# Optimization experiments

Measured on AMD Instinct MI355X. Metric: run time of the kernel, lower is better.

The kernel has to match this reference:

```python
import jax, jax.numpy as jnp
import numpy as np

N = 50000      # nodes
E = 800000     # directed edges (before self-loops)
IN = 128       # in_channels
H = 4          # heads (layers 1,2)
C = 64         # hidden_channels per head
OUT = 512      # out_channels of final Linear
LEAKY_SLOPE = 0.2


def _gat_layer(x, src, dst, n, W, a_src, a_dst, b, concat):
    """PyG GATConv (v1): shared linear, additive attention, segment softmax over dst."""
    heads, ch = a_src.shape
    xl = (x @ W).reshape(n, heads, ch)                       # [N,H,C]
    as_n = jnp.sum(xl * a_src, axis=-1)                      # [N,H] alpha_src per node
    ad_n = jnp.sum(xl * a_dst, axis=-1)                      # [N,H] alpha_dst per node
    logits = jax.nn.leaky_relu(as_n[src] + ad_n[dst], LEAKY_SLOPE)  # [Etot,H]
    m = jax.lax.stop_gradient(jax.ops.segment_max(logits, dst, num_segments=n))
    p = jnp.exp(logits - m[dst])
    denom = jax.ops.segment_sum(p, dst, num_segments=n) + 1e-16
    alpha = p / denom[dst]                                   # segment softmax over incoming edges
    out = jax.ops.segment_sum(xl[src] * alpha[:, :, None], dst, num_segments=n)  # [N,H,C]
    out = out.reshape(n, heads * ch) if concat else out.mean(axis=1)
    return out + b


def setup_inputs() -> dict:
    key = jax.random.key(0)
    ks = jax.random.split(key, 16)

    def gl(k, shape, fan_in):
        return jax.random.normal(k, shape, dtype=jnp.float32) * np.float32(1.0 / np.sqrt(fan_in))

    x = jax.random.normal(ks[0], (N, IN), dtype=jnp.float32)
    edge_index = jax.random.randint(ks[1], (2, E), 0, N, dtype=jnp.int32)

    inp = {
        "x": x,
        "edge_index": edge_index,
        # layer 1: in -> H*C (concat)
        "W1": gl(ks[2], (IN, H * C), IN),
        "a_src1": gl(ks[3], (H, C), C),
        "a_dst1": gl(ks[4], (H, C), C),
        "b1": jnp.zeros((H * C,), jnp.float32),
        # layer 2: H*C -> H*C (concat)
        "W2": gl(ks[5], (H * C, H * C), H * C),
        "a_src2": gl(ks[6], (H, C), C),
        "a_dst2": gl(ks[7], (H, C), C),
        "b2": jnp.zeros((H * C,), jnp.float32),
        # layer 3: H*C -> C (1 head, no concat)
        "W3": gl(ks[8], (H * C, C), H * C),
        "a_src3": gl(ks[9], (1, C), C),
        "a_dst3": gl(ks[10], (1, C), C),
        "b3": jnp.zeros((C,), jnp.float32),
        # final fc: C -> OUT
        "Wfc": gl(ks[11], (C, OUT), C),
        "bfc": jnp.zeros((OUT,), jnp.float32),
    }
    return inp


def reference(x, edge_index, W1, a_src1, a_dst1, b1, W2, a_src2, a_dst2, b2,
              W3, a_src3, a_dst3, b3, Wfc, bfc):
    n = x.shape[0]
    loop = jnp.arange(n, dtype=edge_index.dtype)             # PyG GATConv adds self-loops
    src = jnp.concatenate([edge_index[0], loop])
    dst = jnp.concatenate([edge_index[1], loop])

    h = jax.nn.relu(_gat_layer(x, src, dst, n, W1, a_src1, a_dst1, b1, True))
    h = jax.nn.relu(_gat_layer(h, src, dst, n, W2, a_src2, a_dst2, b2, True))
    h = jax.nn.relu(_gat_layer(h, src, dst, n, W3, a_src3, a_dst3, b3, False))
    return jax.nn.relu(h @ Wfc + bfc)                        # [N, OUT]
```

## Files before the change

kernel.cpp:

```cpp
#include <hip/hip_runtime.h>
#include <cstdint>
#include <cstddef>

typedef unsigned short ushort_t;
typedef __bf16 bf16x8 __attribute__((ext_vector_type(8)));
typedef float f32x4 __attribute__((ext_vector_type(4)));

__device__ __forceinline__ float b2f(ushort_t u) {
    return __uint_as_float(((unsigned int)u) << 16);
}
__device__ __forceinline__ ushort_t f2b(float f) {
    __bf16 h = (__bf16)f;
    return *(ushort_t*)&h;
}
__device__ __forceinline__ float lo16(unsigned int u) { return __uint_as_float(u << 16); }
__device__ __forceinline__ float hi16(unsigned int u) { return __uint_as_float(u & 0xffff0000u); }
__device__ __forceinline__ unsigned int pack2(float a, float b) {
    return ((unsigned int)f2b(b) << 16) | (unsigned int)f2b(a);
}

__device__ __forceinline__ void tr_seg(int id, const float* __restrict__ W,
                                       ushort_t* __restrict__ WT, int K, int N2) {
    int n = id / K, k = id - n * K;
    WT[id] = f2b(W[k * N2 + n]);
}
__global__ __launch_bounds__(256) void transpose_all_kernel(const float* __restrict__ W1,
                                                            const float* __restrict__ W2,
                                                            const float* __restrict__ W3,
                                                            const float* __restrict__ Wfc,
                                                            ushort_t* __restrict__ W1T,
                                                            ushort_t* __restrict__ W2T,
                                                            ushort_t* __restrict__ W3T,
                                                            ushort_t* __restrict__ WfcT) {
    int id = blockIdx.x * 256 + threadIdx.x;
    if (id < 32768) { tr_seg(id, W1, W1T, 128, 256); return; }
    id -= 32768;
    if (id < 65536) { tr_seg(id, W2, W2T, 256, 256); return; }
    id -= 65536;
    if (id < 16384) { tr_seg(id, W3, W3T, 256, 64); return; }
    id -= 16384;
    if (id < 32768) { tr_seg(id, Wfc, WfcT, 64, 512); return; }
}

__global__ __launch_bounds__(256) void xb_kernel(const float* __restrict__ x,
                                                 ushort_t* __restrict__ xb, int total8) {
    int id = blockIdx.x * 256 + threadIdx.x;
    if (id >= total8) return;
    const float* g = x + (size_t)id * 8;
    float4 f0 = *(const float4*)g;
    float4 f1 = *(const float4*)(g + 4);
    uint4 o;
    o.x = pack2(f0.x, f0.y); o.y = pack2(f0.z, f0.w);
    o.z = pack2(f1.x, f1.y); o.w = pack2(f1.z, f1.w);
    ((uint4*)xb)[id] = o;
}

__global__ __launch_bounds__(256) void degree_kernel(const int* __restrict__ ei_dst,
                                                     int* __restrict__ deg, int E, int Etot) {
    int e = blockIdx.x * 256 + threadIdx.x;
    if (e >= Etot) return;
    int d = (e < E) ? ei_dst[e] : (e - E);
    atomicAdd(&deg[d], 1);
}

__global__ __launch_bounds__(256) void partial_sum_kernel(const int* __restrict__ deg,
                                                          int* __restrict__ bsum, int n) {
    __shared__ int ws[4];
    int t = threadIdx.x;
    int i = blockIdx.x * 256 + t;
    int v = (i < n) ? deg[i] : 0;
#pragma unroll
    for (int off = 32; off; off >>= 1) v += __shfl_xor(v, off, 64);
    if ((t & 63) == 0) ws[t >> 6] = v;
    __syncthreads();
    if (t == 0) bsum[blockIdx.x] = ws[0] + ws[1] + ws[2] + ws[3];
}

__global__ __launch_bounds__(256) void scan_bsum_kernel(const int* __restrict__ bsum,
                                                        int* __restrict__ boff,
                                                        int* __restrict__ rowoff,
                                                        int nblk, int n) {
    __shared__ int sm[256];
    int t = threadIdx.x;
    int v = (t < nblk) ? bsum[t] : 0;
    sm[t] = v;
    __syncthreads();
#pragma unroll
    for (int off = 1; off < 256; off <<= 1) {
        int u = (t >= off) ? sm[t - off] : 0;
        __syncthreads();
        sm[t] += u;
        __syncthreads();
    }
    if (t < nblk) boff[t] = sm[t] - v;
    if (t == 255) rowoff[n] = sm[255];
}

__global__ __launch_bounds__(256) void block_scan_kernel(const int* __restrict__ deg,
                                                         const int* __restrict__ boff,
                                                         int* __restrict__ rowoff,
                                                         int* __restrict__ cursor, int n) {
    __shared__ int sm[256];
    int t = threadIdx.x;
    int i = blockIdx.x * 256 + t;
    int v = (i < n) ? deg[i] : 0;
    sm[t] = v;
    __syncthreads();
#pragma unroll
    for (int off = 1; off < 256; off <<= 1) {
        int u = (t >= off) ? sm[t - off] : 0;
        __syncthreads();
        sm[t] += u;
        __syncthreads();
    }
    if (i < n) {
        int r = boff[blockIdx.x] + sm[t] - v;
        rowoff[i] = r;
        cursor[i] = r;
    }
}

__global__ __launch_bounds__(256) void scatter_kernel(const int* __restrict__ ei_src,
                                                      const int* __restrict__ ei_dst,
                                                      int* __restrict__ cursor,
                                                      int* __restrict__ ssrc, int E, int Etot) {
    int e = blockIdx.x * 256 + threadIdx.x;
    if (e >= Etot) return;
    int s, d;
    if (e < E) { s = ei_src[e]; d = ei_dst[e]; } else { s = d = e - E; }
    int pos = atomicAdd(&cursor[d], 1);
    ssrc[pos] = s;
}

template <int EPI>
__global__ __launch_bounds__(256) void gemm128_mfma(const ushort_t* __restrict__ A,
                                                    const ushort_t* __restrict__ WT,
                                                    float* __restrict__ C,
                                                    ushort_t* __restrict__ Cb,
                                                    const float* __restrict__ bias,
                                                    int M, int K, int N2) {
    __shared__ ushort_t sA[128 * 32];
    __shared__ ushort_t sB[128 * 32];
    const int tid = threadIdx.x;
    const int wv = tid >> 6, lane = tid & 63;
    const int wr = wv >> 1, wc = wv & 1;
    const int quad = lane >> 4, l16 = lane & 15;
    const int bm = blockIdx.x * 128, bn = blockIdx.y * 128;
    const int sr0 = tid >> 2, sc = (tid & 3) * 8;
    const int sr1 = sr0 + 64;
    f32x4 acc[4][4] = {};

    int ga0 = bm + sr0; ga0 = ga0 < M ? ga0 : M - 1;
    int ga1 = bm + sr1; ga1 = ga1 < M ? ga1 : M - 1;
    const ushort_t* pa0 = A + (size_t)ga0 * K + sc;
    const ushort_t* pa1 = A + (size_t)ga1 * K + sc;
    const ushort_t* pb0 = WT + (size_t)(bn + sr0) * K + sc;
    const ushort_t* pb1 = WT + (size_t)(bn + sr1) * K + sc;

    for (int k0 = 0; k0 < K; k0 += 32) {
        *(float4*)(sA + sr0 * 32 + sc) = *(const float4*)(pa0 + k0);
        *(float4*)(sA + sr1 * 32 + sc) = *(const float4*)(pa1 + k0);
        *(float4*)(sB + sr0 * 32 + sc) = *(const float4*)(pb0 + k0);
        *(float4*)(sB + sr1 * 32 + sc) = *(const float4*)(pb1 + k0);
        __syncthreads();

        bf16x8 af[4], bfr[4];
#pragma unroll
        for (int m = 0; m < 4; m++)
            af[m] = *(const bf16x8*)(sA + (wr * 64 + m * 16 + l16) * 32 + quad * 8);
#pragma unroll
        for (int n = 0; n < 4; n++)
            bfr[n] = *(const bf16x8*)(sB + (wc * 64 + n * 16 + l16) * 32 + quad * 8);
#pragma unroll
        for (int m = 0; m < 4; m++)
#pragma unroll
            for (int n = 0; n < 4; n++)
                acc[m][n] = __builtin_amdgcn_mfma_f32_16x16x32_bf16(af[m], bfr[n], acc[m][n], 0, 0, 0);
        __syncthreads();
    }

#pragma unroll
    for (int n = 0; n < 4; n++) {
        int col = bn + wc * 64 + n * 16 + l16;
        float bv = (EPI == 1) ? bias[col] : 0.f;
#pragma unroll
        for (int m = 0; m < 4; m++) {
#pragma unroll
            for (int r = 0; r < 4; r++) {
                int row = bm + wr * 64 + m * 16 + quad * 4 + r;
                if (row < M) {
                    float v = acc[m][n][r];
                    if (EPI == 1) {
                        v += bv;
                        v = v > 0.f ? v : 0.f;
                        C[(size_t)row * N2 + col] = v;
                    } else {
                        Cb[(size_t)row * N2 + col] = f2b(v);
                    }
                }
            }
        }
    }
}

__global__ __launch_bounds__(256) void gemm64_mfma(const ushort_t* __restrict__ A,
                                                   const ushort_t* __restrict__ WT,
                                                   ushort_t* __restrict__ Cb,
                                                   int M, int K, int N2) {
    __shared__ ushort_t sA[64 * 32];
    __shared__ ushort_t sB[64 * 32];
    const int tid = threadIdx.x;
    const int wv = tid >> 6, lane = tid & 63;
    const int quad = lane >> 4, l16 = lane & 15;
    const int bm = blockIdx.x * 64;
    const int srow = tid >> 2, skof = (tid & 3) * 8;
    f32x4 acc[4] = {};

    int gm = bm + srow;
    gm = gm < M ? gm : M - 1;
    const ushort_t* pa = A + (size_t)gm * K + skof;
    const ushort_t* pb = WT + (size_t)srow * K + skof;

    for (int k0 = 0; k0 < K; k0 += 32) {
        *(float4*)(sA + srow * 32 + skof) = *(const float4*)(pa + k0);
        *(float4*)(sB + srow * 32 + skof) = *(const float4*)(pb + k0);
        __syncthreads();

        bf16x8 af = *(const bf16x8*)(sA + (wv * 16 + l16) * 32 + quad * 8);
#pragma unroll
        for (int j = 0; j < 4; j++) {
            bf16x8 bf = *(const bf16x8*)(sB + (j * 16 + l16) * 32 + quad * 8);
            acc[j] = __builtin_amdgcn_mfma_f32_16x16x32_bf16(af, bf, acc[j], 0, 0, 0);
        }
        __syncthreads();
    }

#pragma unroll
    for (int j = 0; j < 4; j++) {
        int col = j * 16 + l16;
#pragma unroll
        for (int r = 0; r < 4; r++) {
            int row = bm + wv * 16 + quad * 4 + r;
            if (row < M) Cb[(size_t)row * N2 + col] = f2b(acc[j][r]);
        }
    }
}

template <int CH>
__global__ __launch_bounds__(256) void attn_kernel(const ushort_t* __restrict__ xl,
                                                   const float* __restrict__ a_src,
                                                   const float* __restrict__ a_dst,
                                                   float* __restrict__ as_n,
                                                   float* __restrict__ ad_n, int N) {
    int n = blockIdx.x * 4 + (threadIdx.x >> 6);
    int lane = threadIdx.x & 63;
    if (n >= N) return;
    if (CH == 256) {
        ushort4 u = ((const ushort4*)xl)[(size_t)n * 64 + lane];
        float4 av = ((const float4*)a_src)[lane];
        float4 dv = ((const float4*)a_dst)[lane];
        float x0 = b2f(u.x), x1 = b2f(u.y), x2 = b2f(u.z), x3 = b2f(u.w);
        float s = x0 * av.x + x1 * av.y + x2 * av.z + x3 * av.w;
        float d = x0 * dv.x + x1 * dv.y + x2 * dv.z + x3 * dv.w;
#pragma unroll
        for (int off = 8; off; off >>= 1) {
            s += __shfl_xor(s, off, 64);
            d += __shfl_xor(d, off, 64);
        }
        if ((lane & 15) == 0) {
            int h = lane >> 4;
            as_n[n * 4 + h] = s;
            ad_n[n * 4 + h] = d;
        }
    } else {
        float xv = b2f(xl[(size_t)n * 64 + lane]);
        float s = xv * a_src[lane];
        float d = xv * a_dst[lane];
#pragma unroll
        for (int off = 32; off; off >>= 1) {
            s += __shfl_xor(s, off, 64);
            d += __shfl_xor(d, off, 64);
        }
        if (lane == 0) { as_n[n] = s; ad_n[n] = d; }
    }
}

template <int CH>
__global__ __launch_bounds__(256) void aggregate_kernel(const ushort_t* __restrict__ xl,
                                                        const float* __restrict__ as_n,
                                                        const float* __restrict__ ad_n,
                                                        const int* __restrict__ rowoff,
                                                        const int* __restrict__ ssrc,
                                                        const float* __restrict__ bias,
                                                        ushort_t* __restrict__ hout, int N) {
    const int tid = threadIdx.x;
    const int wv = tid >> 6, lane = tid & 63;
    const uint4* xv = (const uint4*)xl;
    if (CH == 256) {
        const int hw = lane >> 5, l32 = lane & 31;
        const int dd = blockIdx.x * 8 + wv * 2 + hw;
        if (dd >= N) return;
        const int h = l32 >> 3;
        const int r0 = rowoff[dd], r1 = rowoff[dd + 1];
        const float adv = ad_n[dd * 4 + h];
        float a0 = 0, a1 = 0, a2 = 0, a3 = 0, a4 = 0, a5 = 0, a6 = 0, a7 = 0, den = 0;
        for (int i = r0; i < r1; i += 8) {
            int s[8];
            float g[8];
            uint4 u[8];
#pragma unroll
            for (int j = 0; j < 8; j++) {
                int t = i + j;
                s[j] = ssrc[t < r1 ? t : r0];
            }
#pragma unroll
            for (int j = 0; j < 8; j++) g[j] = as_n[s[j] * 4 + h];
#pragma unroll
            for (int j = 0; j < 8; j++) u[j] = xv[(size_t)s[j] * 32 + l32];
#pragma unroll
            for (int j = 0; j < 8; j++) {
                float lg = g[j] + adv;
                lg = lg > 0.f ? lg : 0.2f * lg;
                float p = (i + j < r1) ? __expf(lg) : 0.f;
                den += p;
                a0 += p * lo16(u[j].x); a1 += p * hi16(u[j].x);
                a2 += p * lo16(u[j].y); a3 += p * hi16(u[j].y);
                a4 += p * lo16(u[j].z); a5 += p * hi16(u[j].z);
                a6 += p * lo16(u[j].w); a7 += p * hi16(u[j].w);
            }
        }
        float di = 1.f / (den + 1e-16f);
        float4 b0 = ((const float4*)bias)[l32 * 2];
        float4 b1 = ((const float4*)bias)[l32 * 2 + 1];
        float v0 = a0 * di + b0.x, v1 = a1 * di + b0.y;
        float v2 = a2 * di + b0.z, v3 = a3 * di + b0.w;
        float v4 = a4 * di + b1.x, v5 = a5 * di + b1.y;
        float v6 = a6 * di + b1.z, v7 = a7 * di + b1.w;
        v0 = v0 > 0.f ? v0 : 0.f; v1 = v1 > 0.f ? v1 : 0.f;
        v2 = v2 > 0.f ? v2 : 0.f; v3 = v3 > 0.f ? v3 : 0.f;
        v4 = v4 > 0.f ? v4 : 0.f; v5 = v5 > 0.f ? v5 : 0.f;
        v6 = v6 > 0.f ? v6 : 0.f; v7 = v7 > 0.f ? v7 : 0.f;
        uint4 o;
        o.x = pack2(v0, v1); o.y = pack2(v2, v3);
        o.z = pack2(v4, v5); o.w = pack2(v6, v7);
        ((uint4*)hout)[(size_t)dd * 32 + l32] = o;
    } else {
        const int grp = lane >> 3, l8 = lane & 7;
        const int dd = blockIdx.x * 32 + wv * 8 + grp;
        if (dd >= N) return;
        const int r0 = rowoff[dd], r1 = rowoff[dd + 1];
        const float adv = ad_n[dd];
        float a0 = 0, a1 = 0, a2 = 0, a3 = 0, a4 = 0, a5 = 0, a6 = 0, a7 = 0, den = 0;
        for (int i = r0; i < r1; i += 8) {
            int s[8];
            float g[8];
            uint4 u[8];
#pragma unroll
            for (int j = 0; j < 8; j++) {
                int t = i + j;
                s[j] = ssrc[t < r1 ? t : r0];
            }
#pragma unroll
            for (int j = 0; j < 8; j++) g[j] = as_n[s[j]];
#pragma unroll
            for (int j = 0; j < 8; j++) u[j] = xv[(size_t)s[j] * 8 + l8];
#pragma unroll
            for (int j = 0; j < 8; j++) {
                float lg = g[j] + adv;
                lg = lg > 0.f ? lg : 0.2f * lg;
                float p = (i + j < r1) ? __expf(lg) : 0.f;
                den += p;
                a0 += p * lo16(u[j].x); a1 += p * hi16(u[j].x);
                a2 += p * lo16(u[j].y); a3 += p * hi16(u[j].y);
                a4 += p * lo16(u[j].z); a5 += p * hi16(u[j].z);
                a6 += p * lo16(u[j].w); a7 += p * hi16(u[j].w);
            }
        }
        float di = 1.f / (den + 1e-16f);
        float4 b0 = ((const float4*)bias)[l8 * 2];
        float4 b1 = ((const float4*)bias)[l8 * 2 + 1];
        float v0 = a0 * di + b0.x, v1 = a1 * di + b0.y;
        float v2 = a2 * di + b0.z, v3 = a3 * di + b0.w;
        float v4 = a4 * di + b1.x, v5 = a5 * di + b1.y;
        float v6 = a6 * di + b1.z, v7 = a7 * di + b1.w;
        v0 = v0 > 0.f ? v0 : 0.f; v1 = v1 > 0.f ? v1 : 0.f;
        v2 = v2 > 0.f ? v2 : 0.f; v3 = v3 > 0.f ? v3 : 0.f;
        v4 = v4 > 0.f ? v4 : 0.f; v5 = v5 > 0.f ? v5 : 0.f;
        v6 = v6 > 0.f ? v6 : 0.f; v7 = v7 > 0.f ? v7 : 0.f;
        uint4 o;
        o.x = pack2(v0, v1); o.y = pack2(v2, v3);
        o.z = pack2(v4, v5); o.w = pack2(v6, v7);
        ((uint4*)hout)[(size_t)dd * 8 + l8] = o;
    }
}

extern "C" void kernel_launch(void* const* d_in, const int* in_sizes, int n_in,
                              void* d_out, int out_size, void* d_ws, size_t ws_size,
                              hipStream_t stream) {
    const int N = in_sizes[0] / 128;
    const int E = in_sizes[1] / 2;
    const int Etot = E + N;

    const float* x = (const float*)d_in[0];
    const int* ei = (const int*)d_in[1];
    const int* ei_src = ei;
    const int* ei_dst = ei + E;
    float* out = (float*)d_out;

    const float* as1 = (const float*)d_in[3];
    const float* ad1 = (const float*)d_in[4];
    const float* b1  = (const float*)d_in[5];
    const float* as2 = (const float*)d_in[7];
    const float* ad2 = (const float*)d_in[8];
    const float* b2  = (const float*)d_in[9];
    const float* as3 = (const float*)d_in[11];
    const float* ad3 = (const float*)d_in[12];
    const float* b3  = (const float*)d_in[13];
    const float* bfc = (const float*)d_in[15];

    ushort_t* bufX = (ushort_t*)d_ws;
    ushort_t* bufH = bufX + (size_t)N * 256;
    ushort_t* W1T  = bufH + (size_t)N * 256;
    ushort_t* W2T  = W1T + 32768;
    ushort_t* W3T  = W2T + 65536;
    ushort_t* WfcT = W3T + 16384;
    float* asn = (float*)(WfcT + 32768);
    float* adn = asn + (size_t)N * 4;
    int* deg    = (int*)(adn + (size_t)N * 4);
    int* rowoff = deg + N;
    int* cursor = rowoff + N + 1;
    int* ssrc   = cursor + N;
    int* bsum   = ssrc + Etot;
    int* boff   = bsum + 256;
    ushort_t* xb = (ushort_t*)(boff + 256);

    transpose_all_kernel<<<576, 256, 0, stream>>>((const float*)d_in[2], (const float*)d_in[6],
                                                  (const float*)d_in[10], (const float*)d_in[14],
                                                  W1T, W2T, W3T, WfcT);
    xb_kernel<<<(N * 16 + 255) / 256, 256, 0, stream>>>(x, xb, N * 16);

    hipMemsetAsync(deg, 0, (size_t)N * sizeof(int), stream);
    int eb = (Etot + 255) / 256;
    degree_kernel<<<eb, 256, 0, stream>>>(ei_dst, deg, E, Etot);
    const int NBLK = (N + 255) / 256;
    partial_sum_kernel<<<NBLK, 256, 0, stream>>>(deg, bsum, N);
    scan_bsum_kernel<<<1, 256, 0, stream>>>(bsum, boff, rowoff, NBLK, N);
    block_scan_kernel<<<NBLK, 256, 0, stream>>>(deg, boff, rowoff, cursor, N);
    scatter_kernel<<<eb, 256, 0, stream>>>(ei_src, ei_dst, cursor, ssrc, E, Etot);

    const int MB128 = (N + 127) / 128;
    const int MB64 = (N + 63) / 64;
    int nb4 = (N + 3) / 4;
    int nb8 = (N + 7) / 8;
    int nb32 = (N + 31) / 32;

    gemm128_mfma<0><<<dim3(MB128, 2), 256, 0, stream>>>(xb, W1T, nullptr, bufX, nullptr, N, 128, 256);
    attn_kernel<256><<<nb4, 256, 0, stream>>>(bufX, as1, ad1, asn, adn, N);
    aggregate_kernel<256><<<nb8, 256, 0, stream>>>(bufX, asn, adn, rowoff, ssrc, b1, bufH, N);

    gemm128_mfma<0><<<dim3(MB128, 2), 256, 0, stream>>>(bufH, W2T, nullptr, bufX, nullptr, N, 256, 256);
    attn_kernel<256><<<nb4, 256, 0, stream>>>(bufX, as2, ad2, asn, adn, N);
    aggregate_kernel<256><<<nb8, 256, 0, stream>>>(bufX, asn, adn, rowoff, ssrc, b2, bufH, N);

    gemm64_mfma<<<dim3(MB64, 1), 256, 0, stream>>>(bufH, W3T, bufX, N, 256, 64);
    attn_kernel<64><<<nb4, 256, 0, stream>>>(bufX, as3, ad3, asn, adn, N);
    aggregate_kernel<64><<<nb32, 256, 0, stream>>>(bufX, asn, adn, rowoff, ssrc, b3, bufH, N);

    gemm128_mfma<1><<<dim3(MB128, 4), 256, 0, stream>>>(bufH, WfcT, out, nullptr, bfc, N, 64, 512);
}
```

Baseline: 505.2 us.

## Fuse attention scores into GEMM epilogues and fold fp32->bf16 cast into GEMM staging

```diff
diff --git a/kernel.cpp b/kernel.cpp
--- a/kernel.cpp
+++ b/kernel.cpp
@@ -17,6 +17,18 @@
 __device__ __forceinline__ float hi16(unsigned int u) { return __uint_as_float(u & 0xffff0000u); }
 __device__ __forceinline__ unsigned int pack2(float a, float b) {
     return ((unsigned int)f2b(b) << 16) | (unsigned int)f2b(a);
+}
+
+__device__ __forceinline__ void stage8(const float* __restrict__ g, ushort_t* s) {
+    float4 f0 = *(const float4*)g;
+    float4 f1 = *(const float4*)(g + 4);
+    union { ushort_t u[8]; uint4 v; } t;
+    t.u[0] = f2b(f0.x); t.u[1] = f2b(f0.y); t.u[2] = f2b(f0.z); t.u[3] = f2b(f0.w);
+    t.u[4] = f2b(f1.x); t.u[5] = f2b(f1.y); t.u[6] = f2b(f1.z); t.u[7] = f2b(f1.w);
+    *(uint4*)s = t.v;
+}
+__device__ __forceinline__ void stage8(const ushort_t* __restrict__ g, ushort_t* s) {
+    *(float4*)s = *(const float4*)g;
 }
 
 __device__ __forceinline__ void tr_seg(int id, const float* __restrict__ W,
@@ -31,8 +43,10 @@
                                                             ushort_t* __restrict__ W1T,
                                                             ushort_t* __restrict__ W2T,
                                                             ushort_t* __restrict__ W3T,
-                                                            ushort_t* __restrict__ WfcT) {
+                                                            ushort_t* __restrict__ WfcT,
+                                                            int* __restrict__ deg, int n) {
     int id = blockIdx.x * 256 + threadIdx.x;
+    if (id < n) deg[id] = 0;
     if (id < 32768) { tr_seg(id, W1, W1T, 128, 256); return; }
     id -= 32768;
     if (id < 65536) { tr_seg(id, W2, W2T, 256, 256); return; }
@@ -40,19 +54,6 @@
     if (id < 16384) { tr_seg(id, W3, W3T, 256, 64); return; }
     id -= 16384;
     if (id < 32768) { tr_seg(id, Wfc, WfcT, 64, 512); return; }
-}
-
-__global__ __launch_bounds__(256) void xb_kernel(const float* __restrict__ x,
-                                                 ushort_t* __restrict__ xb, int total8) {
-    int id = blockIdx.x * 256 + threadIdx.x;
-    if (id >= total8) return;
-    const float* g = x + (size_t)id * 8;
-    float4 f0 = *(const float4*)g;
-    float4 f1 = *(const float4*)(g + 4);
-    uint4 o;
-    o.x = pack2(f0.x, f0.y); o.y = pack2(f0.z, f0.w);
-    o.z = pack2(f1.x, f1.y); o.w = pack2(f1.z, f1.w);
-    ((uint4*)xb)[id] = o;
 }
 
 __global__ __launch_bounds__(256) void degree_kernel(const int* __restrict__ ei_dst,
@@ -132,12 +133,16 @@
     ssrc[pos] = s;
 }
 
-template <int EPI>
-__global__ __launch_bounds__(256) void gemm128_mfma(const ushort_t* __restrict__ A,
+template <typename TA, int EPI>
+__global__ __launch_bounds__(256) void gemm128_mfma(const TA* __restrict__ A,
                                                     const ushort_t* __restrict__ WT,
                                                     float* __restrict__ C,
                                                     ushort_t* __restrict__ Cb,
                                                     const float* __restrict__ bias,
+                                                    const float* __restrict__ a_src,
+                                                    const float* __restrict__ a_dst,
+                                                    float* __restrict__ as_n,
+                                                    float* __restrict__ ad_n,
                                                     int M, int K, int N2) {
     __shared__ ushort_t sA[128 * 32];
     __shared__ ushort_t sB[128 * 32];
@@ -152,16 +157,16 @@
 
     int ga0 = bm + sr0; ga0 = ga0 < M ? ga0 : M - 1;
     int ga1 = bm + sr1; ga1 = ga1 < M ? ga1 : M - 1;
-    const ushort_t* pa0 = A + (size_t)ga0 * K + sc;
-    const ushort_t* pa1 = A + (size_t)ga1 * K + sc;
+    const TA* pa0 = A + (size_t)ga0 * K + sc;
+    const TA* pa1 = A + (size_t)ga1 * K + sc;
     const ushort_t* pb0 = WT + (size_t)(bn + sr0) * K + sc;
     const ushort_t* pb1 = WT + (size_t)(bn + sr1) * K + sc;
 
     for (int k0 = 0; k0 < K; k0 += 32) {
-        *(float4*)(sA + sr0 * 32 + sc) = *(const float4*)(pa0 + k0);
-        *(float4*)(sA + sr1 * 32 + sc) = *(const float4*)(pa1 + k0);
-        *(float4*)(sB + sr0 * 32 + sc) = *(const float4*)(pb0 + k0);
-        *(float4*)(sB + sr1 * 32 + sc) = *(const float4*)(pb1 + k0);
+        stage8(pa0 + k0, sA + sr0 * 32 + sc);
+        stage8(pa1 + k0, sA + sr1 * 32 + sc);
+        stage8(pb0 + k0, sB + sr0 * 32 + sc);
+        stage8(pb1 + k0, sB + sr1 * 32 + sc);
         __syncthreads();
 
         bf16x8 af[4], bfr[4];
@@ -201,11 +206,56 @@
             }
         }
     }
+
+    if (EPI == 2) {
+        const int head = blockIdx.y * 2 + wc;
+        float asv[4], adv[4];
+#pragma unroll
+        for (int n = 0; n < 4; n++) {
+            asv[n] = a_src[head * 64 + n * 16 + l16];
+            adv[n] = a_dst[head * 64 + n * 16 + l16];
+        }
+        float ps[4][4] = {}, pd[4][4] = {};
+#pragma unroll
+        for (int n = 0; n < 4; n++)
+#pragma unroll
+            for (int m = 0; m < 4; m++)
+#pragma unroll
+                for (int r = 0; r < 4; r++) {
+                    ps[m][r] += acc[m][n][r] * asv[n];
+                    pd[m][r] += acc[m][n][r] * adv[n];
+                }
+#pragma unroll
+        for (int off = 1; off < 16; off <<= 1)
+#pragma unroll
+            for (int m = 0; m < 4; m++)
+#pragma unroll
+                for (int r = 0; r < 4; r++) {
+                    ps[m][r] += __shfl_xor(ps[m][r], off, 64);
+                    pd[m][r] += __shfl_xor(pd[m][r], off, 64);
+                }
+        if (l16 == 0) {
+#pragma unroll
+            for (int m = 0; m < 4; m++)
+#pragma unroll
+                for (int r = 0; r < 4; r++) {
+                    int row = bm + wr * 64 + m * 16 + quad * 4 + r;
+                    if (row < M) {
+                        as_n[row * 4 + head] = ps[m][r];
+                        ad_n[row * 4 + head] = pd[m][r];
+                    }
+                }
+        }
+    }
 }
 
 __global__ __launch_bounds__(256) void gemm64_mfma(const ushort_t* __restrict__ A,
                                                    const ushort_t* __restrict__ WT,
                                                    ushort_t* __restrict__ Cb,
+                                                   const float* __restrict__ a_src,
+                                                   const float* __restrict__ a_dst,
+                                                   float* __restrict__ as_n,
+                                                   float* __restrict__ ad_n,
                                                    int M, int K, int N2) {
     __shared__ ushort_t sA[64 * 32];
     __shared__ ushort_t sB[64 * 32];
@@ -244,44 +294,37 @@
             if (row < M) Cb[(size_t)row * N2 + col] = f2b(acc[j][r]);
         }
     }
-}
-
-template <int CH>
-__global__ __launch_bounds__(256) void attn_kernel(const ushort_t* __restrict__ xl,
-                                                   const float* __restrict__ a_src,
-                                                   const float* __restrict__ a_dst,
-                                                   float* __restrict__ as_n,
-                                                   float* __restrict__ ad_n, int N) {
-    int n = blockIdx.x * 4 + (threadIdx.x >> 6);
-    int lane = threadIdx.x & 63;
-    if (n >= N) return;
-    if (CH == 256) {
-        ushort4 u = ((const ushort4*)xl)[(size_t)n * 64 + lane];
-        float4 av = ((const float4*)a_src)[lane];
-        float4 dv = ((const float4*)a_dst)[lane];
-        float x0 = b2f(u.x), x1 = b2f(u.y), x2 = b2f(u.z), x3 = b2f(u.w);
-        float s = x0 * av.x + x1 * av.y + x2 * av.z + x3 * av.w;
-        float d = x0 * dv.x + x1 * dv.y + x2 * dv.z + x3 * dv.w;
-#pragma unroll
-        for (int off = 8; off; off >>= 1) {
-            s += __shfl_xor(s, off, 64);
-            d += __shfl_xor(d, off, 64);
-        }
-        if ((lane & 15) == 0) {
-            int h = lane >> 4;
-            as_n[n * 4 + h] = s;
-            ad_n[n * 4 + h] = d;
-        }
-    } else {
-        float xv = b2f(xl[(size_t)n * 64 + lane]);
-        float s = xv * a_src[lane];
-        float d = xv * a_dst[lane];
-#pragma unroll
-        for (int off = 32; off; off >>= 1) {
-            s += __shfl_xor(s, off, 64);
-            d += __shfl_xor(d, off, 64);
-        }
-        if (lane == 0) { as_n[n] = s; ad_n[n] = d; }
+
+    float asv[4], adv[4];
+#pragma unroll
+    for (int j = 0; j < 4; j++) {
+        asv[j] = a_src[j * 16 + l16];
+        adv[j] = a_dst[j * 16 + l16];
+    }
+    float ps[4] = {}, pd[4] = {};
+#pragma unroll
+    for (int j = 0; j < 4; j++)
+#pragma unroll
+        for (int r = 0; r < 4; r++) {
+            ps[r] += acc[j][r] * asv[j];
+            pd[r] += acc[j][r] * adv[j];
+        }
+#pragma unroll
+    for (int off = 1; off < 16; off <<= 1)
+#pragma unroll
+        for (int r = 0; r < 4; r++) {
+            ps[r] += __shfl_xor(ps[r], off, 64);
+            pd[r] += __shfl_xor(pd[r], off, 64);
+        }
+    if (l16 == 0) {
+#pragma unroll
+        for (int r = 0; r < 4; r++) {
+            int row = bm + wv * 16 + quad * 4 + r;
+            if (row < M) {
+                as_n[row] = ps[r];
+                ad_n[row] = pd[r];
+            }
+        }
     }
 }
 
@@ -432,14 +475,11 @@
     int* ssrc   = cursor + N;
     int* bsum   = ssrc + Etot;
     int* boff   = bsum + 256;
-    ushort_t* xb = (ushort_t*)(boff + 256);
 
     transpose_all_kernel<<<576, 256, 0, stream>>>((const float*)d_in[2], (const float*)d_in[6],
                                                   (const float*)d_in[10], (const float*)d_in[14],
-                                                  W1T, W2T, W3T, WfcT);
-    xb_kernel<<<(N * 16 + 255) / 256, 256, 0, stream>>>(x, xb, N * 16);
-
-    hipMemsetAsync(deg, 0, (size_t)N * sizeof(int), stream);
+                                                  W1T, W2T, W3T, WfcT, deg, N);
+
     int eb = (Etot + 255) / 256;
     degree_kernel<<<eb, 256, 0, stream>>>(ei_dst, deg, E, Etot);
     const int NBLK = (N + 255) / 256;
@@ -450,21 +490,20 @@
 
     const int MB128 = (N + 127) / 128;
     const int MB64 = (N + 63) / 64;
-    int nb4 = (N + 3) / 4;
     int nb8 = (N + 7) / 8;
     int nb32 = (N + 31) / 32;
 
-    gemm128_mfma<0><<<dim3(MB128, 2), 256, 0, stream>>>(xb, W1T, nullptr, bufX, nullptr, N, 128, 256);
-    attn_kernel<256><<<nb4, 256, 0, stream>>>(bufX, as1, ad1, asn, adn, N);
+    gemm128_mfma<float, 2><<<dim3(MB128, 2), 256, 0, stream>>>(
+        x, W1T, nullptr, bufX, nullptr, as1, ad1, asn, adn, N, 128, 256);
     aggregate_kernel<256><<<nb8, 256, 0, stream>>>(bufX, asn, adn, rowoff, ssrc, b1, bufH, N);
 
-    gemm128_mfma<0><<<dim3(MB128, 2), 256, 0, stream>>>(bufH, W2T, nullptr, bufX, nullptr, N, 256, 256);
-    attn_kernel<256><<<nb4, 256, 0, stream>>>(bufX, as2, ad2, asn, adn, N);
+    gemm128_mfma<ushort_t, 2><<<dim3(MB128, 2), 256, 0, stream>>>(
+        bufH, W2T, nullptr, bufX, nullptr, as2, ad2, asn, adn, N, 256, 256);
     aggregate_kernel<256><<<nb8, 256, 0, stream>>>(bufX, asn, adn, rowoff, ssrc, b2, bufH, N);
 
-    gemm64_mfma<<<dim3(MB64, 1), 256, 0, stream>>>(bufH, W3T, bufX, N, 256, 64);
-    attn_kernel<64><<<nb4, 256, 0, stream>>>(bufX, as3, ad3, asn, adn, N);
+    gemm64_mfma<<<dim3(MB64, 1), 256, 0, stream>>>(bufH, W3T, bufX, as3, ad3, asn, adn, N, 256, 64);
     aggregate_kernel<64><<<nb32, 256, 0, stream>>>(bufX, asn, adn, rowoff, ssrc, b3, bufH, N);
 
-    gemm128_mfma<1><<<dim3(MB128, 4), 256, 0, stream>>>(bufH, WfcT, out, nullptr, bfc, N, 64, 512);
-}
+    gemm128_mfma<ushort_t, 1><<<dim3(MB128, 4), 256, 0, stream>>>(
+        bufH, WfcT, out, nullptr, bfc, nullptr, nullptr, nullptr, nullptr, N, 64, 512);
+}
```

Result: faster. 483.3 us (-4.3%).
